# Kernel optimization log

Measured on AMD Instinct MI355X. Metric: run time of the kernel, lower is better.

Reference implementation:

```python
import jax, jax.numpy as jnp
import numpy as np

N = 6144      # nodes
NFEAT = 512
NHID = 256
NHEADS = 4
DHEAD = NHID // NHEADS  # 64
NEMBED = 128
NEG_INF = -9e15
LRELU_ALPHA = 0.2


def setup_inputs() -> dict:
    key = jax.random.key(0)
    k = jax.random.split(key, 8)
    x = jax.random.normal(k[0], (N, NFEAT), dtype=jnp.float32)
    adj = (jax.random.uniform(k[1], (N, N)) < 0.01).astype(jnp.int32)
    # per-head GAT params, packed over heads
    W = jax.random.normal(k[2], (NHEADS, NFEAT, DHEAD), dtype=jnp.float32) * 0.05
    a_src = jax.random.normal(k[3], (NHEADS, DHEAD), dtype=jnp.float32) * 0.05
    a_dst = jax.random.normal(k[4], (NHEADS, DHEAD), dtype=jnp.float32) * 0.05
    # output linear (init.normal_ std=0.05 per reset_parameters)
    lin_w = jax.random.normal(k[5], (NEMBED, NHID), dtype=jnp.float32) * 0.05
    lin_b = jnp.zeros((NEMBED,), dtype=jnp.float32)
    return {"x": x, "adj": adj, "W": W, "a_src": a_src, "a_dst": a_dst,
            "lin_w": lin_w, "lin_b": lin_b}


def _gat_forward(x, adj, W, a_src, a_dst, lin_w, lin_b):
    # Wh: [H, N, D]
    Wh = jnp.einsum('nf,hfd->hnd', x, W)
    # attention logits e_ij = leakyrelu(a_src.Wh_i + a_dst.Wh_j): [H, N, N]
    s = jnp.einsum('hnd,hd->hn', Wh, a_src)   # source term per node
    t = jnp.einsum('hnd,hd->hn', Wh, a_dst)   # target term per node
    e = s[:, :, None] + t[:, None, :]
    e = jax.nn.leaky_relu(e, negative_slope=LRELU_ALPHA)
    # mask by adjacency, softmax over neighbors
    e = jnp.where(adj[None, :, :] > 0, e, NEG_INF)
    attn = jax.nn.softmax(e, axis=-1)
    # aggregate and per-head ELU (concat=True GAT layer)
    h = jnp.einsum('hnm,hmd->hnd', attn, Wh)
    h = jax.nn.elu(h)
    # concat heads -> [N, NHID]
    h = jnp.transpose(h, (1, 0, 2)).reshape(N, NHID)
    # dropout is identity in eval mode; linear + ELU
    out = jax.nn.elu(h @ lin_w.T + lin_b)
    return out


def reference(x, adj, W, a_src, a_dst, lin_w, lin_b):
    return _gat_forward(x, adj, W, a_src, a_dst, lin_w, lin_b)
```

## Files before the change

### kernel.cpp

```cpp
#include <hip/hip_runtime.h>
#include <hip/hip_bf16.h>
#include <math.h>

#define N_NODES 6144
#define NFEAT 512
#define NHID 256
#define NHEADS 4
#define DHEAD 64
#define NEMBED 128
#define LRELU_ALPHA 0.2f
#define MAXC 256
#define ASTRIDE 20

typedef __attribute__((ext_vector_type(8))) __bf16 bfrag;
typedef __attribute__((ext_vector_type(4))) float f32x4;

static __device__ __forceinline__ unsigned short f2bf(float f) {
    unsigned u = __float_as_uint(f);
    unsigned r = (u + 0x7FFFu + ((u >> 16) & 1u)) >> 16;
    return (unsigned short)r;
}
static __device__ __forceinline__ float bf2f(unsigned short b) {
    return __uint_as_float((unsigned)b << 16);
}
static __device__ __forceinline__ void split1(float v, unsigned short& h, unsigned short& l) {
    h = f2bf(v);
    l = f2bf(v - bf2f(h));
}
static __device__ __forceinline__ float bfLo(unsigned u) { return __uint_as_float(u << 16); }
static __device__ __forceinline__ float bfHi(unsigned u) { return __uint_as_float(u & 0xffff0000u); }

__global__ __launch_bounds__(256) void gemm_scan(const float* __restrict__ x,
                                                 const float* __restrict__ W,
                                                 const float* __restrict__ a_src,
                                                 const float* __restrict__ a_dst,
                                                 const int* __restrict__ adj,
                                                 unsigned short* __restrict__ Whb,
                                                 float* __restrict__ s_arr,
                                                 float* __restrict__ t_arr,
                                                 int* __restrict__ cnt_g,
                                                 unsigned short* __restrict__ nbr_g) {
    __shared__ unsigned short Ah[64][32];
    __shared__ unsigned short Al[64][32];
    __shared__ unsigned short Bh[64][32];
    __shared__ unsigned short Bl[64][32];
    __shared__ int scnt;
    const int tid = threadIdx.x;

    if (blockIdx.y < NHEADS) {
        const int h = blockIdx.y;
        const int row0 = blockIdx.x * 64;
        const int w = tid >> 6;
        const int lane = tid & 63;
        const int g = lane >> 4;
        const int r = lane & 15;
        const float* Bp = W + (size_t)h * NFEAT * DHEAD;

        f32x4 acc[4] = {};

        const int ar = tid >> 2, akq = (tid & 3) * 8;
        const int bkk = tid >> 3, bnq = tid & 7;
        const int bks = bkk ^ ((bnq & 3) << 3);

        for (int k0 = 0; k0 < NFEAT; k0 += 32) {
            const float4 av0 = *(const float4*)(x + (size_t)(row0 + ar) * NFEAT + k0 + akq);
            const float4 av1 = *(const float4*)(x + (size_t)(row0 + ar) * NFEAT + k0 + akq + 4);
            ushort4 h0, l0, h1, l1;
            split1(av0.x, h0.x, l0.x); split1(av0.y, h0.y, l0.y);
            split1(av0.z, h0.z, l0.z); split1(av0.w, h0.w, l0.w);
            split1(av1.x, h1.x, l1.x); split1(av1.y, h1.y, l1.y);
            split1(av1.z, h1.z, l1.z); split1(av1.w, h1.w, l1.w);
            *(ushort4*)&Ah[ar][akq]     = h0;
            *(ushort4*)&Ah[ar][akq + 4] = h1;
            *(ushort4*)&Al[ar][akq]     = l0;
            *(ushort4*)&Al[ar][akq + 4] = l1;
            const float4 bv0 = *(const float4*)(Bp + (size_t)(k0 + bkk) * DHEAD + bnq * 8);
            const float4 bv1 = *(const float4*)(Bp + (size_t)(k0 + bkk) * DHEAD + bnq * 8 + 4);
            {
                unsigned short hh, ll;
                split1(bv0.x, hh, ll); Bh[bnq * 8 + 0][bks] = hh; Bl[bnq * 8 + 0][bks] = ll;
                split1(bv0.y, hh, ll); Bh[bnq * 8 + 1][bks] = hh; Bl[bnq * 8 + 1][bks] = ll;
                split1(bv0.z, hh, ll); Bh[bnq * 8 + 2][bks] = hh; Bl[bnq * 8 + 2][bks] = ll;
                split1(bv0.w, hh, ll); Bh[bnq * 8 + 3][bks] = hh; Bl[bnq * 8 + 3][bks] = ll;
                split1(bv1.x, hh, ll); Bh[bnq * 8 + 4][bks] = hh; Bl[bnq * 8 + 4][bks] = ll;
                split1(bv1.y, hh, ll); Bh[bnq * 8 + 5][bks] = hh; Bl[bnq * 8 + 5][bks] = ll;
                split1(bv1.z, hh, ll); Bh[bnq * 8 + 6][bks] = hh; Bl[bnq * 8 + 6][bks] = ll;
                split1(bv1.w, hh, ll); Bh[bnq * 8 + 7][bks] = hh; Bl[bnq * 8 + 7][bks] = ll;
            }
            __syncthreads();
            const int arow = w * 16 + r;
            const bfrag ah = *(const bfrag*)&Ah[arow][g * 8];
            const bfrag al = *(const bfrag*)&Al[arow][g * 8];
#pragma unroll
            for (int nt = 0; nt < 4; nt++) {
                const int blk = (g ^ ((2 * nt + (r >> 3)) & 3)) * 8;
                const bfrag bh = *(const bfrag*)&Bh[nt * 16 + r][blk];
                const bfrag bl = *(const bfrag*)&Bl[nt * 16 + r][blk];
                acc[nt] = __builtin_amdgcn_mfma_f32_16x16x32_bf16(ah, bh, acc[nt], 0, 0, 0);
                acc[nt] = __builtin_amdgcn_mfma_f32_16x16x32_bf16(ah, bl, acc[nt], 0, 0, 0);
                acc[nt] = __builtin_amdgcn_mfma_f32_16x16x32_bf16(al, bh, acc[nt], 0, 0, 0);
            }
            __syncthreads();
        }
        float asv[4], adv[4];
#pragma unroll
        for (int nt = 0; nt < 4; nt++) {
            asv[nt] = a_src[h * DHEAD + nt * 16 + r];
            adv[nt] = a_dst[h * DHEAD + nt * 16 + r];
        }
        const int mbase = row0 + w * 16 + 4 * g;
#pragma unroll
        for (int q = 0; q < 4; q++) {
            const int m = mbase + q;
#pragma unroll
            for (int nt = 0; nt < 4; nt++)
                Whb[((size_t)h * N_NODES + m) * DHEAD + nt * 16 + r] = f2bf(acc[nt][q]);
            float ps = acc[0][q] * asv[0] + acc[1][q] * asv[1] +
                       acc[2][q] * asv[2] + acc[3][q] * asv[3];
            float pt = acc[0][q] * adv[0] + acc[1][q] * adv[1] +
                       acc[2][q] * adv[2] + acc[3][q] * adv[3];
#pragma unroll
            for (int off = 1; off < 16; off <<= 1) {
                ps += __shfl_xor(ps, off);
                pt += __shfl_xor(pt, off);
            }
            if (r == 0) {
                s_arr[h * N_NODES + m] = ps;
                t_arr[h * N_NODES + m] = pt;
            }
        }
    } else {
        const int rr = (blockIdx.y - NHEADS) * gridDim.x + blockIdx.x;
        const int* arow = adj + (size_t)rr * N_NODES;
        unsigned short* nrow = nbr_g + (size_t)rr * MAXC;
        if (tid == 0) scnt = 0;
        __syncthreads();
#pragma unroll
        for (int it = 0; it < 6; ++it) {
            const int j0 = it * 1024 + tid * 4;
            const int4 v = *(const int4*)(arow + j0);
            const int n = (v.x != 0) + (v.y != 0) + (v.z != 0) + (v.w != 0);
            if (n) {
                int base = atomicAdd(&scnt, n);
                if (v.x) { if (base < MAXC) nrow[base] = (unsigned short)j0; ++base; }
                if (v.y) { if (base < MAXC) nrow[base] = (unsigned short)(j0 + 1); ++base; }
                if (v.z) { if (base < MAXC) nrow[base] = (unsigned short)(j0 + 2); ++base; }
                if (v.w) { if (base < MAXC) nrow[base] = (unsigned short)(j0 + 3); }
            }
        }
        __syncthreads();
        if (tid == 0) cnt_g[rr] = scnt;
    }
}

__global__ __launch_bounds__(256) void attn_agg(const int* __restrict__ adj,
                                                const unsigned short* __restrict__ Whb,
                                                const float* __restrict__ s_arr,
                                                const float* __restrict__ t_arr,
                                                const int* __restrict__ cnt_g,
                                                const unsigned short* __restrict__ nbr_g,
                                                float* __restrict__ hcat) {
    __shared__ unsigned short nbr[MAXC];
    __shared__ float p_s[NHEADS][MAXC];
    const int i = blockIdx.x;
    const int tid = threadIdx.x;
    const int h = tid >> 6;
    const int lane = tid & 63;
    const int q = lane >> 4;
    const int dq = (lane & 15) * 4;
    const int c = cnt_g[i];
    const unsigned short* wp = Whb + (size_t)h * N_NODES * DHEAD;

    float b0[4] = {0.f, 0.f, 0.f, 0.f};
    float l = 1.0f;
    bool combine = true;

    if (c > 0 && c <= MAXC) {
        for (int k = tid; k < c; k += 256) nbr[k] = nbr_g[(size_t)i * MAXC + k];
        __syncthreads();

        const float s_h = s_arr[h * N_NODES + i];
        const float* tp = t_arr + (size_t)h * N_NODES;
        float m = -INFINITY;
        for (int k = lane; k < c; k += 64) {
            float e = s_h + tp[nbr[k]];
            e = e >= 0.0f ? e : LRELU_ALPHA * e;
            p_s[h][k] = e;
            m = fmaxf(m, e);
        }
#pragma unroll
        for (int off = 32; off > 0; off >>= 1) m = fmaxf(m, __shfl_xor(m, off));
        float ls = 0.0f;
        for (int k = lane; k < c; k += 64) {
            const float p = __expf(p_s[h][k] - m);
            p_s[h][k] = p;
            ls += p;
        }
#pragma unroll
        for (int off = 32; off > 0; off >>= 1) ls += __shfl_xor(ls, off);
        l = ls;

        float b1[4] = {0.f, 0.f, 0.f, 0.f};
        float b2[4] = {0.f, 0.f, 0.f, 0.f};
        float b3[4] = {0.f, 0.f, 0.f, 0.f};
        int k = 0;
        for (; k + 16 <= c; k += 16) {
            const int k0 = k + q, k1 = k + 4 + q, k2 = k + 8 + q, k3 = k + 12 + q;
            const int j0 = nbr[k0], j1 = nbr[k1], j2 = nbr[k2], j3 = nbr[k3];
            const float p0 = p_s[h][k0], p1 = p_s[h][k1];
            const float p2 = p_s[h][k2], p3 = p_s[h][k3];
            const uint2 w0 = *(const uint2*)(wp + (size_t)j0 * DHEAD + dq);
            const uint2 w1 = *(const uint2*)(wp + (size_t)j1 * DHEAD + dq);
            const uint2 w2 = *(const uint2*)(wp + (size_t)j2 * DHEAD + dq);
            const uint2 w3 = *(const uint2*)(wp + (size_t)j3 * DHEAD + dq);
            b0[0] += p0 * bfLo(w0.x); b0[1] += p0 * bfHi(w0.x);
            b0[2] += p0 * bfLo(w0.y); b0[3] += p0 * bfHi(w0.y);
            b1[0] += p1 * bfLo(w1.x); b1[1] += p1 * bfHi(w1.x);
            b1[2] += p1 * bfLo(w1.y); b1[3] += p1 * bfHi(w1.y);
            b2[0] += p2 * bfLo(w2.x); b2[1] += p2 * bfHi(w2.x);
            b2[2] += p2 * bfLo(w2.y); b2[3] += p2 * bfHi(w2.y);
            b3[0] += p3 * bfLo(w3.x); b3[1] += p3 * bfHi(w3.x);
            b3[2] += p3 * bfLo(w3.y); b3[3] += p3 * bfHi(w3.y);
        }
        for (; k < c; k += 4) {
            const int kk = k + q;
            const int j = (kk < c) ? nbr[kk] : nbr[k];
            const float p = (kk < c) ? p_s[h][kk] : 0.0f;
            const uint2 w = *(const uint2*)(wp + (size_t)j * DHEAD + dq);
            b0[0] += p * bfLo(w.x); b0[1] += p * bfHi(w.x);
            b0[2] += p * bfLo(w.y); b0[3] += p * bfHi(w.y);
        }
#pragma unroll
        for (int d = 0; d < 4; d++) b0[d] = (b0[d] + b1[d]) + (b2[d] + b3[d]);
    } else if (c == 0) {
        for (int j = q; j < N_NODES; j += 4) {
            const uint2 w = *(const uint2*)(wp + (size_t)j * DHEAD + dq);
            b0[0] += bfLo(w.x); b0[1] += bfHi(w.x);
            b0[2] += bfLo(w.y); b0[3] += bfHi(w.y);
        }
        l = (float)N_NODES;
    } else {
        combine = false;
        const int* arow = adj + (size_t)i * N_NODES;
        const float s_h = s_arr[h * N_NODES + i];
        const float* tp = t_arr + (size_t)h * N_NODES;
        float m = -INFINITY, ll = 0.0f;
        for (int j = 0; j < N_NODES; j++) {
            if (arow[j]) {
                float e = s_h + tp[j];
                e = e >= 0.0f ? e : LRELU_ALPHA * e;
                const float m_new = fmaxf(m, e);
                const float scale = __expf(m - m_new);
                const float p = __expf(e - m_new);
                ll = ll * scale + p;
                const uint2 w = *(const uint2*)(wp + (size_t)j * DHEAD + dq);
                b0[0] = b0[0] * scale + p * bfLo(w.x);
                b0[1] = b0[1] * scale + p * bfHi(w.x);
                b0[2] = b0[2] * scale + p * bfLo(w.y);
                b0[3] = b0[3] * scale + p * bfHi(w.y);
                m = m_new;
            }
        }
        l = ll;
    }

    if (combine) {
#pragma unroll
        for (int d = 0; d < 4; d++) {
            b0[d] += __shfl_xor(b0[d], 16);
            b0[d] += __shfl_xor(b0[d], 32);
        }
    }
    if (lane < 16) {
        float4 hv;
        float* pv = &hv.x;
#pragma unroll
        for (int d = 0; d < 4; d++) {
            float v = b0[d] / l;
            pv[d] = v > 0.0f ? v : expm1f(v);
        }
        *(float4*)(hcat + (size_t)i * NHID + h * DHEAD + dq) = hv;
    }
}

__global__ __launch_bounds__(256) void out_gemm(const float* __restrict__ hcat,
                                                const float* __restrict__ lin_w,
                                                const float* __restrict__ lin_b,
                                                float* __restrict__ out) {
    __shared__ float As[64][ASTRIDE * 4];
    __shared__ float Bs[16][64];
    const int tid = threadIdx.x;
    const int tx = tid & 15;
    const int ty = tid >> 4;
    const int row0 = blockIdx.x * 64;
    const int c0 = blockIdx.y * 64;

    float acc[4][4] = {};

    for (int k0 = 0; k0 < NHID; k0 += 16) {
        {
            const int r = tid >> 2, kq = tid & 3;
            const float4 v = *(const float4*)(hcat + (size_t)(row0 + r) * NHID + k0 + kq * 4);
            *(float4*)&As[r][kq * 4] = v;
        }
        {
            const int cc = tid & 63, kq = tid >> 6;
            const float4 v = *(const float4*)(lin_w + (size_t)(c0 + cc) * NHID + k0 + kq * 4);
            Bs[kq * 4 + 0][cc] = v.x;
            Bs[kq * 4 + 1][cc] = v.y;
            Bs[kq * 4 + 2][cc] = v.z;
            Bs[kq * 4 + 3][cc] = v.w;
        }
        __syncthreads();
#pragma unroll
        for (int kk = 0; kk < 16; kk++) {
            float a[4], b[4];
#pragma unroll
            for (int i = 0; i < 4; i++) a[i] = As[ty * 4 + i][kk];
#pragma unroll
            for (int j = 0; j < 4; j++) b[j] = Bs[kk][tx * 4 + j];
#pragma unroll
            for (int i = 0; i < 4; i++)
#pragma unroll
                for (int j = 0; j < 4; j++) acc[i][j] += a[i] * b[j];
        }
        __syncthreads();
    }
#pragma unroll
    for (int i = 0; i < 4; i++) {
        const int row = row0 + ty * 4 + i;
        float v[4];
#pragma unroll
        for (int j = 0; j < 4; j++) {
            const int col = c0 + tx * 4 + j;
            float val = acc[i][j] + lin_b[col];
            v[j] = val > 0.0f ? val : expm1f(val);
        }
        *(float4*)(out + (size_t)row * NEMBED + c0 + tx * 4) =
            make_float4(v[0], v[1], v[2], v[3]);
    }
}

extern "C" void kernel_launch(void* const* d_in, const int* in_sizes, int n_in,
                              void* d_out, int out_size, void* d_ws, size_t ws_size,
                              hipStream_t stream) {
    const float* x     = (const float*)d_in[0];
    const int*   adj   = (const int*)d_in[1];
    const float* W     = (const float*)d_in[2];
    const float* a_src = (const float*)d_in[3];
    const float* a_dst = (const float*)d_in[4];
    const float* lin_w = (const float*)d_in[5];
    const float* lin_b = (const float*)d_in[6];
    float* out = (float*)d_out;

    unsigned short* Whb = (unsigned short*)d_ws;
    float* s    = (float*)(Whb + (size_t)NHEADS * N_NODES * DHEAD);
    float* t    = s + (size_t)NHEADS * N_NODES;
    float* hcat = t + (size_t)NHEADS * N_NODES;
    int* cnt_g  = (int*)(hcat + (size_t)N_NODES * NHID);
    unsigned short* nbr_g = (unsigned short*)(cnt_g + N_NODES);

    gemm_scan<<<dim3(96, NHEADS + 64), 256, 0, stream>>>(
        x, W, a_src, a_dst, adj, Whb, s, t, cnt_g, nbr_g);
    attn_agg<<<N_NODES, 256, 0, stream>>>(adj, Whb, s, t, cnt_g, nbr_g, hcat);
    out_gemm<<<dim3(N_NODES / 64, NEMBED / 64), 256, 0, stream>>>(hcat, lin_w, lin_b, out);
}
```

Before: 275.7 us.

## Fuse adjacency scan into attention kernel, drop global neighbor lists

Moves the per-row adjacency scan from the GEMM kernel into the attention/aggregation kernel, building the neighbor list directly in shared memory. This removes the global write and reread of neighbor indices and counts. In exchange, the adjacency read no longer overlaps with the Wh GEMM, and the GEMM launch now has only 384 blocks.

```diff
diff --git a/kernel.cpp b/kernel.cpp
--- a/kernel.cpp
+++ b/kernel.cpp
@@ -30,155 +30,142 @@
 static __device__ __forceinline__ float bfLo(unsigned u) { return __uint_as_float(u << 16); }
 static __device__ __forceinline__ float bfHi(unsigned u) { return __uint_as_float(u & 0xffff0000u); }
 
-__global__ __launch_bounds__(256) void gemm_scan(const float* __restrict__ x,
-                                                 const float* __restrict__ W,
-                                                 const float* __restrict__ a_src,
-                                                 const float* __restrict__ a_dst,
-                                                 const int* __restrict__ adj,
-                                                 unsigned short* __restrict__ Whb,
-                                                 float* __restrict__ s_arr,
-                                                 float* __restrict__ t_arr,
-                                                 int* __restrict__ cnt_g,
-                                                 unsigned short* __restrict__ nbr_g) {
+__global__ __launch_bounds__(256) void gemm_k1(const float* __restrict__ x,
+                                               const float* __restrict__ W,
+                                               const float* __restrict__ a_src,
+                                               const float* __restrict__ a_dst,
+                                               unsigned short* __restrict__ Whb,
+                                               float* __restrict__ s_arr,
+                                               float* __restrict__ t_arr) {
     __shared__ unsigned short Ah[64][32];
     __shared__ unsigned short Al[64][32];
     __shared__ unsigned short Bh[64][32];
     __shared__ unsigned short Bl[64][32];
-    __shared__ int scnt;
     const int tid = threadIdx.x;
 
-    if (blockIdx.y < NHEADS) {
-        const int h = blockIdx.y;
-        const int row0 = blockIdx.x * 64;
-        const int w = tid >> 6;
-        const int lane = tid & 63;
-        const int g = lane >> 4;
-        const int r = lane & 15;
-        const float* Bp = W + (size_t)h * NFEAT * DHEAD;
-
-        f32x4 acc[4] = {};
-
-        const int ar = tid >> 2, akq = (tid & 3) * 8;
-        const int bkk = tid >> 3, bnq = tid & 7;
-        const int bks = bkk ^ ((bnq & 3) << 3);
-
-        for (int k0 = 0; k0 < NFEAT; k0 += 32) {
-            const float4 av0 = *(const float4*)(x + (size_t)(row0 + ar) * NFEAT + k0 + akq);
-            const float4 av1 = *(const float4*)(x + (size_t)(row0 + ar) * NFEAT + k0 + akq + 4);
-            ushort4 h0, l0, h1, l1;
-            split1(av0.x, h0.x, l0.x); split1(av0.y, h0.y, l0.y);
-            split1(av0.z, h0.z, l0.z); split1(av0.w, h0.w, l0.w);
-            split1(av1.x, h1.x, l1.x); split1(av1.y, h1.y, l1.y);
-            split1(av1.z, h1.z, l1.z); split1(av1.w, h1.w, l1.w);
-            *(ushort4*)&Ah[ar][akq]     = h0;
-            *(ushort4*)&Ah[ar][akq + 4] = h1;
-            *(ushort4*)&Al[ar][akq]     = l0;
-            *(ushort4*)&Al[ar][akq + 4] = l1;
-            const float4 bv0 = *(const float4*)(Bp + (size_t)(k0 + bkk) * DHEAD + bnq * 8);
-            const float4 bv1 = *(const float4*)(Bp + (size_t)(k0 + bkk) * DHEAD + bnq * 8 + 4);
-            {
-                unsigned short hh, ll;
-                split1(bv0.x, hh, ll); Bh[bnq * 8 + 0][bks] = hh; Bl[bnq * 8 + 0][bks] = ll;
-                split1(bv0.y, hh, ll); Bh[bnq * 8 + 1][bks] = hh; Bl[bnq * 8 + 1][bks] = ll;
-                split1(bv0.z, hh, ll); Bh[bnq * 8 + 2][bks] = hh; Bl[bnq * 8 + 2][bks] = ll;
-                split1(bv0.w, hh, ll); Bh[bnq * 8 + 3][bks] = hh; Bl[bnq * 8 + 3][bks] = ll;
-                split1(bv1.x, hh, ll); Bh[bnq * 8 + 4][bks] = hh; Bl[bnq * 8 + 4][bks] = ll;
-                split1(bv1.y, hh, ll); Bh[bnq * 8 + 5][bks] = hh; Bl[bnq * 8 + 5][bks] = ll;
-                split1(bv1.z, hh, ll); Bh[bnq * 8 + 6][bks] = hh; Bl[bnq * 8 + 6][bks] = ll;
-                split1(bv1.w, hh, ll); Bh[bnq * 8 + 7][bks] = hh; Bl[bnq * 8 + 7][bks] = ll;
-            }
-            __syncthreads();
-            const int arow = w * 16 + r;
-            const bfrag ah = *(const bfrag*)&Ah[arow][g * 8];
-            const bfrag al = *(const bfrag*)&Al[arow][g * 8];
-#pragma unroll
-            for (int nt = 0; nt < 4; nt++) {
-                const int blk = (g ^ ((2 * nt + (r >> 3)) & 3)) * 8;
-                const bfrag bh = *(const bfrag*)&Bh[nt * 16 + r][blk];
-                const bfrag bl = *(const bfrag*)&Bl[nt * 16 + r][blk];
-                acc[nt] = __builtin_amdgcn_mfma_f32_16x16x32_bf16(ah, bh, acc[nt], 0, 0, 0);
-                acc[nt] = __builtin_amdgcn_mfma_f32_16x16x32_bf16(ah, bl, acc[nt], 0, 0, 0);
-                acc[nt] = __builtin_amdgcn_mfma_f32_16x16x32_bf16(al, bh, acc[nt], 0, 0, 0);
-            }
-            __syncthreads();
-        }
-        float asv[4], adv[4];
+    const int h = blockIdx.y;
+    const int row0 = blockIdx.x * 64;
+    const int w = tid >> 6;
+    const int lane = tid & 63;
+    const int g = lane >> 4;
+    const int r = lane & 15;
+    const float* Bp = W + (size_t)h * NFEAT * DHEAD;
+
+    f32x4 acc[4] = {};
+
+    const int ar = tid >> 2, akq = (tid & 3) * 8;
+    const int bkk = tid >> 3, bnq = tid & 7;
+    const int bks = bkk ^ ((bnq & 3) << 3);
+
+    for (int k0 = 0; k0 < NFEAT; k0 += 32) {
+        const float4 av0 = *(const float4*)(x + (size_t)(row0 + ar) * NFEAT + k0 + akq);
+        const float4 av1 = *(const float4*)(x + (size_t)(row0 + ar) * NFEAT + k0 + akq + 4);
+        ushort4 h0, l0, h1, l1;
+        split1(av0.x, h0.x, l0.x); split1(av0.y, h0.y, l0.y);
+        split1(av0.z, h0.z, l0.z); split1(av0.w, h0.w, l0.w);
+        split1(av1.x, h1.x, l1.x); split1(av1.y, h1.y, l1.y);
+        split1(av1.z, h1.z, l1.z); split1(av1.w, h1.w, l1.w);
+        *(ushort4*)&Ah[ar][akq]     = h0;
+        *(ushort4*)&Ah[ar][akq + 4] = h1;
+        *(ushort4*)&Al[ar][akq]     = l0;
+        *(ushort4*)&Al[ar][akq + 4] = l1;
+        const float4 bv0 = *(const float4*)(Bp + (size_t)(k0 + bkk) * DHEAD + bnq * 8);
+        const float4 bv1 = *(const float4*)(Bp + (size_t)(k0 + bkk) * DHEAD + bnq * 8 + 4);
+        {
+            unsigned short hh, ll;
+            split1(bv0.x, hh, ll); Bh[bnq * 8 + 0][bks] = hh; Bl[bnq * 8 + 0][bks] = ll;
+            split1(bv0.y, hh, ll); Bh[bnq * 8 + 1][bks] = hh; Bl[bnq * 8 + 1][bks] = ll;
+            split1(bv0.z, hh, ll); Bh[bnq * 8 + 2][bks] = hh; Bl[bnq * 8 + 2][bks] = ll;
+            split1(bv0.w, hh, ll); Bh[bnq * 8 + 3][bks] = hh; Bl[bnq * 8 + 3][bks] = ll;
+            split1(bv1.x, hh, ll); Bh[bnq * 8 + 4][bks] = hh; Bl[bnq * 8 + 4][bks] = ll;
+            split1(bv1.y, hh, ll); Bh[bnq * 8 + 5][bks] = hh; Bl[bnq * 8 + 5][bks] = ll;
+            split1(bv1.z, hh, ll); Bh[bnq * 8 + 6][bks] = hh; Bl[bnq * 8 + 6][bks] = ll;
+            split1(bv1.w, hh, ll); Bh[bnq * 8 + 7][bks] = hh; Bl[bnq * 8 + 7][bks] = ll;
+        }
+        __syncthreads();
+        const int arow = w * 16 + r;
+        const bfrag ah = *(const bfrag*)&Ah[arow][g * 8];
+        const bfrag al = *(const bfrag*)&Al[arow][g * 8];
 #pragma unroll
         for (int nt = 0; nt < 4; nt++) {
-            asv[nt] = a_src[h * DHEAD + nt * 16 + r];
-            adv[nt] = a_dst[h * DHEAD + nt * 16 + r];
-        }
-        const int mbase = row0 + w * 16 + 4 * g;
-#pragma unroll
-        for (int q = 0; q < 4; q++) {
-            const int m = mbase + q;
-#pragma unroll
-            for (int nt = 0; nt < 4; nt++)
-                Whb[((size_t)h * N_NODES + m) * DHEAD + nt * 16 + r] = f2bf(acc[nt][q]);
-            float ps = acc[0][q] * asv[0] + acc[1][q] * asv[1] +
-                       acc[2][q] * asv[2] + acc[3][q] * asv[3];
-            float pt = acc[0][q] * adv[0] + acc[1][q] * adv[1] +
-                       acc[2][q] * adv[2] + acc[3][q] * adv[3];
-#pragma unroll
-            for (int off = 1; off < 16; off <<= 1) {
-                ps += __shfl_xor(ps, off);
-                pt += __shfl_xor(pt, off);
-            }
-            if (r == 0) {
-                s_arr[h * N_NODES + m] = ps;
-                t_arr[h * N_NODES + m] = pt;
-            }
-        }
-    } else {
-        const int rr = (blockIdx.y - NHEADS) * gridDim.x + blockIdx.x;
-        const int* arow = adj + (size_t)rr * N_NODES;
-        unsigned short* nrow = nbr_g + (size_t)rr * MAXC;
-        if (tid == 0) scnt = 0;
+            const int blk = (g ^ ((2 * nt + (r >> 3)) & 3)) * 8;
+            const bfrag bh = *(const bfrag*)&Bh[nt * 16 + r][blk];
+            const bfrag bl = *(const bfrag*)&Bl[nt * 16 + r][blk];
+            acc[nt] = __builtin_amdgcn_mfma_f32_16x16x32_bf16(ah, bh, acc[nt], 0, 0, 0);
+            acc[nt] = __builtin_amdgcn_mfma_f32_16x16x32_bf16(ah, bl, acc[nt], 0, 0, 0);
+            acc[nt] = __builtin_amdgcn_mfma_f32_16x16x32_bf16(al, bh, acc[nt], 0, 0, 0);
+        }
         __syncthreads();
-#pragma unroll
-        for (int it = 0; it < 6; ++it) {
-            const int j0 = it * 1024 + tid * 4;
-            const int4 v = *(const int4*)(arow + j0);
-            const int n = (v.x != 0) + (v.y != 0) + (v.z != 0) + (v.w != 0);
-            if (n) {
-                int base = atomicAdd(&scnt, n);
-                if (v.x) { if (base < MAXC) nrow[base] = (unsigned short)j0; ++base; }
-                if (v.y) { if (base < MAXC) nrow[base] = (unsigned short)(j0 + 1); ++base; }
-                if (v.z) { if (base < MAXC) nrow[base] = (unsigned short)(j0 + 2); ++base; }
-                if (v.w) { if (base < MAXC) nrow[base] = (unsigned short)(j0 + 3); }
-            }
-        }
-        __syncthreads();
-        if (tid == 0) cnt_g[rr] = scnt;
-    }
-}
-
-__global__ __launch_bounds__(256) void attn_agg(const int* __restrict__ adj,
-                                                const unsigned short* __restrict__ Whb,
-                                                const float* __restrict__ s_arr,
-                                                const float* __restrict__ t_arr,
-                                                const int* __restrict__ cnt_g,
-                                                const unsigned short* __restrict__ nbr_g,
-                                                float* __restrict__ hcat) {
+    }
+    float asv[4], adv[4];
+#pragma unroll
+    for (int nt = 0; nt < 4; nt++) {
+        asv[nt] = a_src[h * DHEAD + nt * 16 + r];
+        adv[nt] = a_dst[h * DHEAD + nt * 16 + r];
+    }
+    const int mbase = row0 + w * 16 + 4 * g;
+#pragma unroll
+    for (int q = 0; q < 4; q++) {
+        const int m = mbase + q;
+#pragma unroll
+        for (int nt = 0; nt < 4; nt++)
+            Whb[((size_t)h * N_NODES + m) * DHEAD + nt * 16 + r] = f2bf(acc[nt][q]);
+        float ps = acc[0][q] * asv[0] + acc[1][q] * asv[1] +
+                   acc[2][q] * asv[2] + acc[3][q] * asv[3];
+        float pt = acc[0][q] * adv[0] + acc[1][q] * adv[1] +
+                   acc[2][q] * adv[2] + acc[3][q] * adv[3];
+#pragma unroll
+        for (int off = 1; off < 16; off <<= 1) {
+            ps += __shfl_xor(ps, off);
+            pt += __shfl_xor(pt, off);
+        }
+        if (r == 0) {
+            s_arr[h * N_NODES + m] = ps;
+            t_arr[h * N_NODES + m] = pt;
+        }
+    }
+}
+
+__global__ __launch_bounds__(256) void scan_attn(const int* __restrict__ adj,
+                                                 const unsigned short* __restrict__ Whb,
+                                                 const float* __restrict__ s_arr,
+                                                 const float* __restrict__ t_arr,
+                                                 float* __restrict__ hcat) {
     __shared__ unsigned short nbr[MAXC];
     __shared__ float p_s[NHEADS][MAXC];
+    __shared__ int scnt;
     const int i = blockIdx.x;
     const int tid = threadIdx.x;
     const int h = tid >> 6;
     const int lane = tid & 63;
     const int q = lane >> 4;
     const int dq = (lane & 15) * 4;
-    const int c = cnt_g[i];
     const unsigned short* wp = Whb + (size_t)h * N_NODES * DHEAD;
+    const int* arow = adj + (size_t)i * N_NODES;
+
+    if (tid == 0) scnt = 0;
+    __syncthreads();
+#pragma unroll
+    for (int it = 0; it < 6; ++it) {
+        const int j0 = it * 1024 + tid * 4;
+        const int4 v = *(const int4*)(arow + j0);
+        const int n = (v.x != 0) + (v.y != 0) + (v.z != 0) + (v.w != 0);
+        if (n) {
+            int base = atomicAdd(&scnt, n);
+            if (v.x) { if (base < MAXC) nbr[base] = (unsigned short)j0; ++base; }
+            if (v.y) { if (base < MAXC) nbr[base] = (unsigned short)(j0 + 1); ++base; }
+            if (v.z) { if (base < MAXC) nbr[base] = (unsigned short)(j0 + 2); ++base; }
+            if (v.w) { if (base < MAXC) nbr[base] = (unsigned short)(j0 + 3); }
+        }
+    }
+    __syncthreads();
+    const int c = scnt;
 
     float b0[4] = {0.f, 0.f, 0.f, 0.f};
     float l = 1.0f;
     bool combine = true;
 
     if (c > 0 && c <= MAXC) {
-        for (int k = tid; k < c; k += 256) nbr[k] = nbr_g[(size_t)i * MAXC + k];
-        __syncthreads();
-
         const float s_h = s_arr[h * N_NODES + i];
         const float* tp = t_arr + (size_t)h * N_NODES;
         float m = -INFINITY;
@@ -241,7 +228,6 @@
         l = (float)N_NODES;
     } else {
         combine = false;
-        const int* arow = adj + (size_t)i * N_NODES;
         const float s_h = s_arr[h * N_NODES + i];
         const float* tp = t_arr + (size_t)h * N_NODES;
         float m = -INFINITY, ll = 0.0f;
@@ -357,11 +343,8 @@
     float* s    = (float*)(Whb + (size_t)NHEADS * N_NODES * DHEAD);
     float* t    = s + (size_t)NHEADS * N_NODES;
     float* hcat = t + (size_t)NHEADS * N_NODES;
-    int* cnt_g  = (int*)(hcat + (size_t)N_NODES * NHID);
-    unsigned short* nbr_g = (unsigned short*)(cnt_g + N_NODES);
-
-    gemm_scan<<<dim3(96, NHEADS + 64), 256, 0, stream>>>(
-        x, W, a_src, a_dst, adj, Whb, s, t, cnt_g, nbr_g);
-    attn_agg<<<N_NODES, 256, 0, stream>>>(adj, Whb, s, t, cnt_g, nbr_g, hcat);
+
+    gemm_k1<<<dim3(96, NHEADS), 256, 0, stream>>>(x, W, a_src, a_dst, Whb, s, t);
+    scan_attn<<<N_NODES, 256, 0, stream>>>(adj, Whb, s, t, hcat);
     out_gemm<<<dim3(N_NODES / 64, NEMBED / 64), 256, 0, stream>>>(hcat, lin_w, lin_b, out);
 }
```

New measurement: 295.0 us. +7.0%, slower.

## Split fused gemm/scan kernel and remap attention to one wave per node

Applied to the files above, without the earlier changes.

The combined GEMM+adjacency-scan launch is split into two separate kernels, scan_csr and gemm_k1. attn_agg is restructured so each wave handles one node across all four heads, with 16 lanes per head. Neighbour indices are held in registers and broadcast with shuffles, and probabilities are staged in a small LDS buffer, replacing the per-node 256-thread block. This aims to cut block overhead and syncs, at the cost of an extra launch and a fast path limited to at most 128 neighbours; rows with more neighbours go to a serial per-lane fallback.

```diff
diff --git a/kernel.cpp b/kernel.cpp
--- a/kernel.cpp
+++ b/kernel.cpp
@@ -30,126 +30,126 @@
 static __device__ __forceinline__ float bfLo(unsigned u) { return __uint_as_float(u << 16); }
 static __device__ __forceinline__ float bfHi(unsigned u) { return __uint_as_float(u & 0xffff0000u); }
 
-__global__ __launch_bounds__(256) void gemm_scan(const float* __restrict__ x,
-                                                 const float* __restrict__ W,
-                                                 const float* __restrict__ a_src,
-                                                 const float* __restrict__ a_dst,
-                                                 const int* __restrict__ adj,
-                                                 unsigned short* __restrict__ Whb,
-                                                 float* __restrict__ s_arr,
-                                                 float* __restrict__ t_arr,
-                                                 int* __restrict__ cnt_g,
-                                                 unsigned short* __restrict__ nbr_g) {
+__global__ __launch_bounds__(256) void scan_csr(const int* __restrict__ adj,
+                                                int* __restrict__ cnt_g,
+                                                unsigned short* __restrict__ nbr_g) {
+    __shared__ int scnt;
+    const int tid = threadIdx.x;
+    const int r = blockIdx.x;
+    const int* arow = adj + (size_t)r * N_NODES;
+    unsigned short* nrow = nbr_g + (size_t)r * MAXC;
+    if (tid == 0) scnt = 0;
+    __syncthreads();
+#pragma unroll
+    for (int it = 0; it < 6; ++it) {
+        const int j0 = it * 1024 + tid * 4;
+        const int4 v = *(const int4*)(arow + j0);
+        const int n = (v.x != 0) + (v.y != 0) + (v.z != 0) + (v.w != 0);
+        if (n) {
+            int base = atomicAdd(&scnt, n);
+            if (v.x) { if (base < MAXC) nrow[base] = (unsigned short)j0; ++base; }
+            if (v.y) { if (base < MAXC) nrow[base] = (unsigned short)(j0 + 1); ++base; }
+            if (v.z) { if (base < MAXC) nrow[base] = (unsigned short)(j0 + 2); ++base; }
+            if (v.w) { if (base < MAXC) nrow[base] = (unsigned short)(j0 + 3); }
+        }
+    }
+    __syncthreads();
+    if (tid == 0) cnt_g[r] = scnt;
+}
+
+__global__ __launch_bounds__(256) void gemm_k1(const float* __restrict__ x,
+                                               const float* __restrict__ W,
+                                               const float* __restrict__ a_src,
+                                               const float* __restrict__ a_dst,
+                                               unsigned short* __restrict__ Whb,
+                                               float* __restrict__ s_arr,
+                                               float* __restrict__ t_arr) {
     __shared__ unsigned short Ah[64][32];
     __shared__ unsigned short Al[64][32];
     __shared__ unsigned short Bh[64][32];
     __shared__ unsigned short Bl[64][32];
-    __shared__ int scnt;
     const int tid = threadIdx.x;
 
-    if (blockIdx.y < NHEADS) {
-        const int h = blockIdx.y;
-        const int row0 = blockIdx.x * 64;
-        const int w = tid >> 6;
-        const int lane = tid & 63;
-        const int g = lane >> 4;
-        const int r = lane & 15;
-        const float* Bp = W + (size_t)h * NFEAT * DHEAD;
-
-        f32x4 acc[4] = {};
-
-        const int ar = tid >> 2, akq = (tid & 3) * 8;
-        const int bkk = tid >> 3, bnq = tid & 7;
-        const int bks = bkk ^ ((bnq & 3) << 3);
-
-        for (int k0 = 0; k0 < NFEAT; k0 += 32) {
-            const float4 av0 = *(const float4*)(x + (size_t)(row0 + ar) * NFEAT + k0 + akq);
-            const float4 av1 = *(const float4*)(x + (size_t)(row0 + ar) * NFEAT + k0 + akq + 4);
-            ushort4 h0, l0, h1, l1;
-            split1(av0.x, h0.x, l0.x); split1(av0.y, h0.y, l0.y);
-            split1(av0.z, h0.z, l0.z); split1(av0.w, h0.w, l0.w);
-            split1(av1.x, h1.x, l1.x); split1(av1.y, h1.y, l1.y);
-            split1(av1.z, h1.z, l1.z); split1(av1.w, h1.w, l1.w);
-            *(ushort4*)&Ah[ar][akq]     = h0;
-            *(ushort4*)&Ah[ar][akq + 4] = h1;
-            *(ushort4*)&Al[ar][akq]     = l0;
-            *(ushort4*)&Al[ar][akq + 4] = l1;
-            const float4 bv0 = *(const float4*)(Bp + (size_t)(k0 + bkk) * DHEAD + bnq * 8);
-            const float4 bv1 = *(const float4*)(Bp + (size_t)(k0 + bkk) * DHEAD + bnq * 8 + 4);
-            {
-                unsigned short hh, ll;
-                split1(bv0.x, hh, ll); Bh[bnq * 8 + 0][bks] = hh; Bl[bnq * 8 + 0][bks] = ll;
-                split1(bv0.y, hh, ll); Bh[bnq * 8 + 1][bks] = hh; Bl[bnq * 8 + 1][bks] = ll;
-                split1(bv0.z, hh, ll); Bh[bnq * 8 + 2][bks] = hh; Bl[bnq * 8 + 2][bks] = ll;
-                split1(bv0.w, hh, ll); Bh[bnq * 8 + 3][bks] = hh; Bl[bnq * 8 + 3][bks] = ll;
-                split1(bv1.x, hh, ll); Bh[bnq * 8 + 4][bks] = hh; Bl[bnq * 8 + 4][bks] = ll;
-                split1(bv1.y, hh, ll); Bh[bnq * 8 + 5][bks] = hh; Bl[bnq * 8 + 5][bks] = ll;
-                split1(bv1.z, hh, ll); Bh[bnq * 8 + 6][bks] = hh; Bl[bnq * 8 + 6][bks] = ll;
-                split1(bv1.w, hh, ll); Bh[bnq * 8 + 7][bks] = hh; Bl[bnq * 8 + 7][bks] = ll;
-            }
-            __syncthreads();
-            const int arow = w * 16 + r;
-            const bfrag ah = *(const bfrag*)&Ah[arow][g * 8];
-            const bfrag al = *(const bfrag*)&Al[arow][g * 8];
-#pragma unroll
-            for (int nt = 0; nt < 4; nt++) {
-                const int blk = (g ^ ((2 * nt + (r >> 3)) & 3)) * 8;
-                const bfrag bh = *(const bfrag*)&Bh[nt * 16 + r][blk];
-                const bfrag bl = *(const bfrag*)&Bl[nt * 16 + r][blk];
-                acc[nt] = __builtin_amdgcn_mfma_f32_16x16x32_bf16(ah, bh, acc[nt], 0, 0, 0);
-                acc[nt] = __builtin_amdgcn_mfma_f32_16x16x32_bf16(ah, bl, acc[nt], 0, 0, 0);
-                acc[nt] = __builtin_amdgcn_mfma_f32_16x16x32_bf16(al, bh, acc[nt], 0, 0, 0);
-            }
-            __syncthreads();
-        }
-        float asv[4], adv[4];
+    const int h = blockIdx.y;
+    const int row0 = blockIdx.x * 64;
+    const int w = tid >> 6;
+    const int lane = tid & 63;
+    const int g = lane >> 4;
+    const int r = lane & 15;
+    const float* Bp = W + (size_t)h * NFEAT * DHEAD;
+
+    f32x4 acc[4] = {};
+
+    const int ar = tid >> 2, akq = (tid & 3) * 8;
+    const int bkk = tid >> 3, bnq = tid & 7;
+    const int bks = bkk ^ ((bnq & 3) << 3);
+
+    for (int k0 = 0; k0 < NFEAT; k0 += 32) {
+        const float4 av0 = *(const float4*)(x + (size_t)(row0 + ar) * NFEAT + k0 + akq);
+        const float4 av1 = *(const float4*)(x + (size_t)(row0 + ar) * NFEAT + k0 + akq + 4);
+        ushort4 h0, l0, h1, l1;
+        split1(av0.x, h0.x, l0.x); split1(av0.y, h0.y, l0.y);
+        split1(av0.z, h0.z, l0.z); split1(av0.w, h0.w, l0.w);
+        split1(av1.x, h1.x, l1.x); split1(av1.y, h1.y, l1.y);
+        split1(av1.z, h1.z, l1.z); split1(av1.w, h1.w, l1.w);
+        *(ushort4*)&Ah[ar][akq]     = h0;
+        *(ushort4*)&Ah[ar][akq + 4] = h1;
+        *(ushort4*)&Al[ar][akq]     = l0;
+        *(ushort4*)&Al[ar][akq + 4] = l1;
+        const float4 bv0 = *(const float4*)(Bp + (size_t)(k0 + bkk) * DHEAD + bnq * 8);
+        const float4 bv1 = *(const float4*)(Bp + (size_t)(k0 + bkk) * DHEAD + bnq * 8 + 4);
+        {
+            unsigned short hh, ll;
+            split1(bv0.x, hh, ll); Bh[bnq * 8 + 0][bks] = hh; Bl[bnq * 8 + 0][bks] = ll;
+            split1(bv0.y, hh, ll); Bh[bnq * 8 + 1][bks] = hh; Bl[bnq * 8 + 1][bks] = ll;
+            split1(bv0.z, hh, ll); Bh[bnq * 8 + 2][bks] = hh; Bl[bnq * 8 + 2][bks] = ll;
+            split1(bv0.w, hh, ll); Bh[bnq * 8 + 3][bks] = hh; Bl[bnq * 8 + 3][bks] = ll;
+            split1(bv1.x, hh, ll); Bh[bnq * 8 + 4][bks] = hh; Bl[bnq * 8 + 4][bks] = ll;
+            split1(bv1.y, hh, ll); Bh[bnq * 8 + 5][bks] = hh; Bl[bnq * 8 + 5][bks] = ll;
+            split1(bv1.z, hh, ll); Bh[bnq * 8 + 6][bks] = hh; Bl[bnq * 8 + 6][bks] = ll;
+            split1(bv1.w, hh, ll); Bh[bnq * 8 + 7][bks] = hh; Bl[bnq * 8 + 7][bks] = ll;
+        }
+        __syncthreads();
+        const int arow = w * 16 + r;
+        const bfrag ah = *(const bfrag*)&Ah[arow][g * 8];
+        const bfrag al = *(const bfrag*)&Al[arow][g * 8];
 #pragma unroll
         for (int nt = 0; nt < 4; nt++) {
-            asv[nt] = a_src[h * DHEAD + nt * 16 + r];
-            adv[nt] = a_dst[h * DHEAD + nt * 16 + r];
-        }
-        const int mbase = row0 + w * 16 + 4 * g;
-#pragma unroll
-        for (int q = 0; q < 4; q++) {
-            const int m = mbase + q;
-#pragma unroll
-            for (int nt = 0; nt < 4; nt++)
-                Whb[((size_t)h * N_NODES + m) * DHEAD + nt * 16 + r] = f2bf(acc[nt][q]);
-            float ps = acc[0][q] * asv[0] + acc[1][q] * asv[1] +
-                       acc[2][q] * asv[2] + acc[3][q] * asv[3];
-            float pt = acc[0][q] * adv[0] + acc[1][q] * adv[1] +
-                       acc[2][q] * adv[2] + acc[3][q] * adv[3];
-#pragma unroll
-            for (int off = 1; off < 16; off <<= 1) {
-                ps += __shfl_xor(ps, off);
-                pt += __shfl_xor(pt, off);
-            }
-            if (r == 0) {
-                s_arr[h * N_NODES + m] = ps;
-                t_arr[h * N_NODES + m] = pt;
-            }
-        }
-    } else {
-        const int rr = (blockIdx.y - NHEADS) * gridDim.x + blockIdx.x;
-        const int* arow = adj + (size_t)rr * N_NODES;
-        unsigned short* nrow = nbr_g + (size_t)rr * MAXC;
-        if (tid == 0) scnt = 0;
+            const int blk = (g ^ ((2 * nt + (r >> 3)) & 3)) * 8;
+            const bfrag bh = *(const bfrag*)&Bh[nt * 16 + r][blk];
+            const bfrag bl = *(const bfrag*)&Bl[nt * 16 + r][blk];
+            acc[nt] = __builtin_amdgcn_mfma_f32_16x16x32_bf16(ah, bh, acc[nt], 0, 0, 0);
+            acc[nt] = __builtin_amdgcn_mfma_f32_16x16x32_bf16(ah, bl, acc[nt], 0, 0, 0);
+            acc[nt] = __builtin_amdgcn_mfma_f32_16x16x32_bf16(al, bh, acc[nt], 0, 0, 0);
+        }
         __syncthreads();
-#pragma unroll
-        for (int it = 0; it < 6; ++it) {
-            const int j0 = it * 1024 + tid * 4;
-            const int4 v = *(const int4*)(arow + j0);
-            const int n = (v.x != 0) + (v.y != 0) + (v.z != 0) + (v.w != 0);
-            if (n) {
-                int base = atomicAdd(&scnt, n);
-                if (v.x) { if (base < MAXC) nrow[base] = (unsigned short)j0; ++base; }
-                if (v.y) { if (base < MAXC) nrow[base] = (unsigned short)(j0 + 1); ++base; }
-                if (v.z) { if (base < MAXC) nrow[base] = (unsigned short)(j0 + 2); ++base; }
-                if (v.w) { if (base < MAXC) nrow[base] = (unsigned short)(j0 + 3); }
-            }
-        }
-        __syncthreads();
-        if (tid == 0) cnt_g[rr] = scnt;
+    }
+    float asv[4], adv[4];
+#pragma unroll
+    for (int nt = 0; nt < 4; nt++) {
+        asv[nt] = a_src[h * DHEAD + nt * 16 + r];
+        adv[nt] = a_dst[h * DHEAD + nt * 16 + r];
+    }
+    const int mbase = row0 + w * 16 + 4 * g;
+#pragma unroll
+    for (int q = 0; q < 4; q++) {
+        const int m = mbase + q;
+#pragma unroll
+        for (int nt = 0; nt < 4; nt++)
+            Whb[((size_t)h * N_NODES + m) * DHEAD + nt * 16 + r] = f2bf(acc[nt][q]);
+        float ps = acc[0][q] * asv[0] + acc[1][q] * asv[1] +
+                   acc[2][q] * asv[2] + acc[3][q] * asv[3];
+        float pt = acc[0][q] * adv[0] + acc[1][q] * adv[1] +
+                   acc[2][q] * adv[2] + acc[3][q] * adv[3];
+#pragma unroll
+        for (int off = 1; off < 16; off <<= 1) {
+            ps += __shfl_xor(ps, off);
+            pt += __shfl_xor(pt, off);
+        }
+        if (r == 0) {
+            s_arr[h * N_NODES + m] = ps;
+            t_arr[h * N_NODES + m] = pt;
+        }
     }
 }
 
@@ -160,127 +160,156 @@
                                                 const int* __restrict__ cnt_g,
                                                 const unsigned short* __restrict__ nbr_g,
                                                 float* __restrict__ hcat) {
-    __shared__ unsigned short nbr[MAXC];
-    __shared__ float p_s[NHEADS][MAXC];
-    const int i = blockIdx.x;
+    __shared__ float p_lds[4][4][132];
     const int tid = threadIdx.x;
-    const int h = tid >> 6;
+    const int w = tid >> 6;
     const int lane = tid & 63;
-    const int q = lane >> 4;
-    const int dq = (lane & 15) * 4;
+    const int g = lane >> 4;
+    const int r = lane & 15;
+    const int i = blockIdx.x * 4 + w;
     const int c = cnt_g[i];
-    const unsigned short* wp = Whb + (size_t)h * N_NODES * DHEAD;
-
-    float b0[4] = {0.f, 0.f, 0.f, 0.f};
+    const unsigned short* wp = Whb + (size_t)g * N_NODES * DHEAD;
+    const unsigned short* nrow = nbr_g + (size_t)i * MAXC;
+    const int dofs = r * 4;
+
+    float a0[4] = {0.f, 0.f, 0.f, 0.f};
+    float a1[4] = {0.f, 0.f, 0.f, 0.f};
     float l = 1.0f;
-    bool combine = true;
-
-    if (c > 0 && c <= MAXC) {
-        for (int k = tid; k < c; k += 256) nbr[k] = nbr_g[(size_t)i * MAXC + k];
-        __syncthreads();
-
-        const float s_h = s_arr[h * N_NODES + i];
-        const float* tp = t_arr + (size_t)h * N_NODES;
+
+    if (c > 0 && c <= 128) {
+        const int nj0 = nrow[lane];
+        const int nj1 = nrow[64 + lane];
+        const float s_h = s_arr[g * N_NODES + i];
+        const float* tp = t_arr + (size_t)g * N_NODES;
+
+        float ev[8];
         float m = -INFINITY;
-        for (int k = lane; k < c; k += 64) {
-            float e = s_h + tp[nbr[k]];
-            e = e >= 0.0f ? e : LRELU_ALPHA * e;
-            p_s[h][k] = e;
+#pragma unroll
+        for (int it = 0; it < 8; it++) {
+            const int k = r + 16 * it;
+            const int j = (it < 4) ? __shfl(nj0, k) : __shfl(nj1, k - 64);
+            float e = -INFINITY;
+            if (k < c) {
+                e = s_h + tp[j];
+                e = e >= 0.0f ? e : LRELU_ALPHA * e;
+            }
+            ev[it] = e;
             m = fmaxf(m, e);
         }
 #pragma unroll
-        for (int off = 32; off > 0; off >>= 1) m = fmaxf(m, __shfl_xor(m, off));
+        for (int off = 1; off < 16; off <<= 1) m = fmaxf(m, __shfl_xor(m, off));
         float ls = 0.0f;
-        for (int k = lane; k < c; k += 64) {
-            const float p = __expf(p_s[h][k] - m);
-            p_s[h][k] = p;
-            ls += p;
-        }
-#pragma unroll
-        for (int off = 32; off > 0; off >>= 1) ls += __shfl_xor(ls, off);
+#pragma unroll
+        for (int it = 0; it < 8; it++) {
+            const int k = r + 16 * it;
+            if (k < c) {
+                const float p = __expf(ev[it] - m);
+                ls += p;
+                p_lds[w][g][k] = p;
+            }
+        }
+#pragma unroll
+        for (int off = 1; off < 16; off <<= 1) ls += __shfl_xor(ls, off);
         l = ls;
 
-        float b1[4] = {0.f, 0.f, 0.f, 0.f};
-        float b2[4] = {0.f, 0.f, 0.f, 0.f};
-        float b3[4] = {0.f, 0.f, 0.f, 0.f};
-        int k = 0;
-        for (; k + 16 <= c; k += 16) {
-            const int k0 = k + q, k1 = k + 4 + q, k2 = k + 8 + q, k3 = k + 12 + q;
-            const int j0 = nbr[k0], j1 = nbr[k1], j2 = nbr[k2], j3 = nbr[k3];
-            const float p0 = p_s[h][k0], p1 = p_s[h][k1];
-            const float p2 = p_s[h][k2], p3 = p_s[h][k3];
-            const uint2 w0 = *(const uint2*)(wp + (size_t)j0 * DHEAD + dq);
-            const uint2 w1 = *(const uint2*)(wp + (size_t)j1 * DHEAD + dq);
-            const uint2 w2 = *(const uint2*)(wp + (size_t)j2 * DHEAD + dq);
-            const uint2 w3 = *(const uint2*)(wp + (size_t)j3 * DHEAD + dq);
-            b0[0] += p0 * bfLo(w0.x); b0[1] += p0 * bfHi(w0.x);
-            b0[2] += p0 * bfLo(w0.y); b0[3] += p0 * bfHi(w0.y);
-            b1[0] += p1 * bfLo(w1.x); b1[1] += p1 * bfHi(w1.x);
-            b1[2] += p1 * bfLo(w1.y); b1[3] += p1 * bfHi(w1.y);
-            b2[0] += p2 * bfLo(w2.x); b2[1] += p2 * bfHi(w2.x);
-            b2[2] += p2 * bfLo(w2.y); b2[3] += p2 * bfHi(w2.y);
-            b3[0] += p3 * bfLo(w3.x); b3[1] += p3 * bfHi(w3.x);
-            b3[2] += p3 * bfLo(w3.y); b3[3] += p3 * bfHi(w3.y);
-        }
-        for (; k < c; k += 4) {
-            const int kk = k + q;
-            const int j = (kk < c) ? nbr[kk] : nbr[k];
-            const float p = (kk < c) ? p_s[h][kk] : 0.0f;
-            const uint2 w = *(const uint2*)(wp + (size_t)j * DHEAD + dq);
-            b0[0] += p * bfLo(w.x); b0[1] += p * bfHi(w.x);
-            b0[2] += p * bfLo(w.y); b0[3] += p * bfHi(w.y);
-        }
-#pragma unroll
-        for (int d = 0; d < 4; d++) b0[d] = (b0[d] + b1[d]) + (b2[d] + b3[d]);
+        const int c0 = c < 64 ? c : 64;
+        int j = 0;
+        for (; j + 4 <= c0; j += 4) {
+            const int ja = __shfl(nj0, j),     jb = __shfl(nj0, j + 1);
+            const int jc = __shfl(nj0, j + 2), jd = __shfl(nj0, j + 3);
+            const float pa = p_lds[w][g][j],     pb = p_lds[w][g][j + 1];
+            const float pc = p_lds[w][g][j + 2], pd = p_lds[w][g][j + 3];
+            const uint2 wa = *(const uint2*)(wp + (size_t)ja * DHEAD + dofs);
+            const uint2 wb = *(const uint2*)(wp + (size_t)jb * DHEAD + dofs);
+            const uint2 wc = *(const uint2*)(wp + (size_t)jc * DHEAD + dofs);
+            const uint2 wd = *(const uint2*)(wp + (size_t)jd * DHEAD + dofs);
+            a0[0] += pa * bfLo(wa.x); a0[1] += pa * bfHi(wa.x);
+            a0[2] += pa * bfLo(wa.y); a0[3] += pa * bfHi(wa.y);
+            a1[0] += pb * bfLo(wb.x); a1[1] += pb * bfHi(wb.x);
+            a1[2] += pb * bfLo(wb.y); a1[3] += pb * bfHi(wb.y);
+            a0[0] += pc * bfLo(wc.x); a0[1] += pc * bfHi(wc.x);
+            a0[2] += pc * bfLo(wc.y); a0[3] += pc * bfHi(wc.y);
+            a1[0] += pd * bfLo(wd.x); a1[1] += pd * bfHi(wd.x);
+            a1[2] += pd * bfLo(wd.y); a1[3] += pd * bfHi(wd.y);
+        }
+        for (; j < c0; j++) {
+            const int ja = __shfl(nj0, j);
+            const float pa = p_lds[w][g][j];
+            const uint2 wa = *(const uint2*)(wp + (size_t)ja * DHEAD + dofs);
+            a0[0] += pa * bfLo(wa.x); a0[1] += pa * bfHi(wa.x);
+            a0[2] += pa * bfLo(wa.y); a0[3] += pa * bfHi(wa.y);
+        }
+        for (j = 64; j + 2 <= c; j += 2) {
+            const int ja = __shfl(nj1, j - 64), jb = __shfl(nj1, j - 63);
+            const float pa = p_lds[w][g][j], pb = p_lds[w][g][j + 1];
+            const uint2 wa = *(const uint2*)(wp + (size_t)ja * DHEAD + dofs);
+            const uint2 wb = *(const uint2*)(wp + (size_t)jb * DHEAD + dofs);
+            a0[0] += pa * bfLo(wa.x); a0[1] += pa * bfHi(wa.x);
+            a0[2] += pa * bfLo(wa.y); a0[3] += pa * bfHi(wa.y);
+            a1[0] += pb * bfLo(wb.x); a1[1] += pb * bfHi(wb.x);
+            a1[2] += pb * bfLo(wb.y); a1[3] += pb * bfHi(wb.y);
+        }
+        if (j < c) {
+            const int ja = __shfl(nj1, j - 64);
+            const float pa = p_lds[w][g][j];
+            const uint2 wa = *(const uint2*)(wp + (size_t)ja * DHEAD + dofs);
+            a0[0] += pa * bfLo(wa.x); a0[1] += pa * bfHi(wa.x);
+            a0[2] += pa * bfLo(wa.y); a0[3] += pa * bfHi(wa.y);
+        }
     } else if (c == 0) {
-        for (int j = q; j < N_NODES; j += 4) {
-            const uint2 w = *(const uint2*)(wp + (size_t)j * DHEAD + dq);
-            b0[0] += bfLo(w.x); b0[1] += bfHi(w.x);
-            b0[2] += bfLo(w.y); b0[3] += bfHi(w.y);
+        for (int j = 0; j < N_NODES; j++) {
+            const uint2 wv = *(const uint2*)(wp + (size_t)j * DHEAD + dofs);
+            a0[0] += bfLo(wv.x); a0[1] += bfHi(wv.x);
+            a0[2] += bfLo(wv.y); a0[3] += bfHi(wv.y);
         }
         l = (float)N_NODES;
     } else {
-        combine = false;
-        const int* arow = adj + (size_t)i * N_NODES;
-        const float s_h = s_arr[h * N_NODES + i];
-        const float* tp = t_arr + (size_t)h * N_NODES;
+        const float s_h = s_arr[g * N_NODES + i];
+        const float* tp = t_arr + (size_t)g * N_NODES;
         float m = -INFINITY, ll = 0.0f;
-        for (int j = 0; j < N_NODES; j++) {
-            if (arow[j]) {
+        if (c <= MAXC) {
+            for (int k = 0; k < c; k++) {
+                const int j = nrow[k];
                 float e = s_h + tp[j];
                 e = e >= 0.0f ? e : LRELU_ALPHA * e;
-                const float m_new = fmaxf(m, e);
-                const float scale = __expf(m - m_new);
-                const float p = __expf(e - m_new);
-                ll = ll * scale + p;
-                const uint2 w = *(const uint2*)(wp + (size_t)j * DHEAD + dq);
-                b0[0] = b0[0] * scale + p * bfLo(w.x);
-                b0[1] = b0[1] * scale + p * bfHi(w.x);
-                b0[2] = b0[2] * scale + p * bfLo(w.y);
-                b0[3] = b0[3] * scale + p * bfHi(w.y);
-                m = m_new;
+                const float mn = fmaxf(m, e);
+                const float sc = __expf(m - mn), p = __expf(e - mn);
+                ll = ll * sc + p;
+                const uint2 wv = *(const uint2*)(wp + (size_t)j * DHEAD + dofs);
+                a0[0] = a0[0] * sc + p * bfLo(wv.x);
+                a0[1] = a0[1] * sc + p * bfHi(wv.x);
+                a0[2] = a0[2] * sc + p * bfLo(wv.y);
+                a0[3] = a0[3] * sc + p * bfHi(wv.y);
+                m = mn;
             }
+        } else {
+            const int* arow = adj + (size_t)i * N_NODES;
+            for (int j = 0; j < N_NODES; j++) {
+                if (arow[j]) {
+                    float e = s_h + tp[j];
+                    e = e >= 0.0f ? e : LRELU_ALPHA * e;
+                    const float mn = fmaxf(m, e);
+                    const float sc = __expf(m - mn), p = __expf(e - mn);
+                    ll = ll * sc + p;
+                    const uint2 wv = *(const uint2*)(wp + (size_t)j * DHEAD + dofs);
+                    a0[0] = a0[0] * sc + p * bfLo(wv.x);
+                    a0[1] = a0[1] * sc + p * bfHi(wv.x);
+                    a0[2] = a0[2] * sc + p * bfLo(wv.y);
+                    a0[3] = a0[3] * sc + p * bfHi(wv.y);
+                    m = mn;
+                }
+            }
         }
         l = ll;
     }
 
-    if (combine) {
-#pragma unroll
-        for (int d = 0; d < 4; d++) {
-            b0[d] += __shfl_xor(b0[d], 16);
-            b0[d] += __shfl_xor(b0[d], 32);
-        }
-    }
-    if (lane < 16) {
-        float4 hv;
-        float* pv = &hv.x;
-#pragma unroll
-        for (int d = 0; d < 4; d++) {
-            float v = b0[d] / l;
-            pv[d] = v > 0.0f ? v : expm1f(v);
-        }
-        *(float4*)(hcat + (size_t)i * NHID + h * DHEAD + dq) = hv;
-    }
+    float4 hv;
+#pragma unroll
+    for (int d = 0; d < 4; d++) {
+        float v = (a0[d] + a1[d]) / l;
+        (&hv.x)[d] = v > 0.0f ? v : expm1f(v);
+    }
+    *(float4*)(hcat + (size_t)i * NHID + g * DHEAD + dofs) = hv;
 }
 
 __global__ __launch_bounds__(256) void out_gemm(const float* __restrict__ hcat,
@@ -360,8 +389,8 @@
     int* cnt_g  = (int*)(hcat + (size_t)N_NODES * NHID);
     unsigned short* nbr_g = (unsigned short*)(cnt_g + N_NODES);
 
-    gemm_scan<<<dim3(96, NHEADS + 64), 256, 0, stream>>>(
-        x, W, a_src, a_dst, adj, Whb, s, t, cnt_g, nbr_g);
-    attn_agg<<<N_NODES, 256, 0, stream>>>(adj, Whb, s, t, cnt_g, nbr_g, hcat);
+    scan_csr<<<N_NODES, 256, 0, stream>>>(adj, cnt_g, nbr_g);
+    gemm_k1<<<dim3(96, NHEADS), 256, 0, stream>>>(x, W, a_src, a_dst, Whb, s, t);
+    attn_agg<<<N_NODES / 4, 256, 0, stream>>>(adj, Whb, s, t, cnt_g, nbr_g, hcat);
     out_gemm<<<dim3(N_NODES / 64, NEMBED / 64), 256, 0, stream>>>(hcat, lin_w, lin_b, out);
 }
```

After: 296.3 us. +7.5%, slower.
